# Optimization experiments

Hardware: AMD Instinct MI355X
Metric: run time of the kernel (lower is better)

## Reference

```python
import jax, jax.numpy as jnp
import numpy as np

K = 3           # kernel_size
PAD = 1         # padding
HEADS = 6
C = 192
CH = C // HEADS           # channels per head = 32
SCALE = CH ** (-0.5)
KK = K * K                # 9


def unfold3(x):
    # x: [N,C,H,W] -> [N,C,9,H,W] (im2col with k=3, pad=1, stride=1)
    N, c, H, W = x.shape
    xp = jnp.pad(x, ((0, 0), (0, 0), (PAD, PAD), (PAD, PAD)))
    return jnp.stack([xp[:, :, i:i + H, j:j + W] for i in range(K) for j in range(K)], axis=2)


def fold3(y):
    # y: [N,C,9,H,W] -> [N,C,H,W] (scatter-add inverse of unfold3)
    N, c, kk, H, W = y.shape
    out = jnp.zeros((N, c, H + 2 * PAD, W + 2 * PAD), dtype=y.dtype)
    idx = 0
    for i in range(K):
        for j in range(K):
            out = out.at[:, :, i:i + H, j:j + W].add(y[:, :, idx])
            idx += 1
    return out[:, :, PAD:PAD + H, PAD:PAD + W]


def setup_inputs() -> dict:
    key = jax.random.key(0)
    ks = jax.random.split(key, 6)
    N, H, W = 16, 56, 56
    s = 0.02
    return {
        "x": jax.random.normal(ks[0], (N, C, H, W), jnp.float32),
        "Wv": jax.random.normal(ks[1], (C, C), jnp.float32) * s,          # fc (no bias)
        "Wa": jax.random.normal(ks[2], (C, KK * KK * HEADS), jnp.float32) * s,  # fc_att weight
        "ba": jax.random.normal(ks[3], (KK * KK * HEADS,), jnp.float32) * s,
        "Wp": jax.random.normal(ks[4], (C, C), jnp.float32) * s,          # fc_proj weight
        "bp": jax.random.normal(ks[5], (C,), jnp.float32) * s,
    }


def reference(x, Wv, Wa, ba, Wp, bp):
    N, c, H, W = x.shape
    HW = H * W
    # value projection (pointwise linear over channels)
    v = jnp.einsum("nchw,cd->ndhw", x, Wv)
    # unfold values: [N,C,9,H,W] -> [N,heads,ch,9,HW] -> [N,heads,HW,9,ch]
    vu = unfold3(v).reshape(N, HEADS, CH, KK, HW).transpose(0, 1, 4, 3, 2)
    # attention logits from (avg-pooled, here identity since stride=1) input
    att = jnp.einsum("nchw,ck->nhwk", x, Wa) + ba       # [N,H,W,81*heads]
    att = att.reshape(N, HW, HEADS, KK, KK).transpose(0, 2, 1, 3, 4)  # [N,heads,HW,9,9]
    att = jax.nn.softmax(att * SCALE, axis=-1)          # dropout is identity at inference
    # apply per-position 9x9 attention to the 9 gathered neighbors
    out = jnp.einsum("nhpkl,nhplc->nhpkc", att, vu)      # [N,heads,HW,9,ch]
    # fold back: layout (heads, ch, kk) matches unfold layout (C, kk)
    out = out.transpose(0, 1, 4, 3, 2).reshape(N, c, KK, H, W)
    folded = fold3(out)                                  # [N,C,H,W]
    # output projection
    return jnp.einsum("nchw,cd->ndhw", folded, Wp) + bp[None, :, None, None]
```

## Files before the change

kernel.cpp:

```cpp
#include <hip/hip_runtime.h>
#include <hip/hip_bf16.h>
#include <math.h>

#define HW 3136
#define NC 192
#define NHEADS 6
#define IMG 56
#define NATT 486
#define YSTR 768
#define ATT_SCALE 0.17677669529663687f

typedef __attribute__((ext_vector_type(8))) short short8;
typedef __attribute__((ext_vector_type(8))) unsigned short ushort8;
typedef __attribute__((ext_vector_type(4))) float float4v;

__device__ __forceinline__ float bf2f(unsigned short u) {
    unsigned int x = ((unsigned int)u) << 16;
    return __builtin_bit_cast(float, x);
}
__device__ __forceinline__ unsigned short f2bf(float f) {
    __hip_bfloat16 h = __float2bfloat16(f);
    return __builtin_bit_cast(unsigned short, h);
}
__device__ __forceinline__ void gload_lds16(const void* g, void* l) {
    __builtin_amdgcn_global_load_lds((const __attribute__((address_space(1))) void*)g,
                                     (__attribute__((address_space(3))) void*)l, 16, 0, 0);
}

__global__ __launch_bounds__(256) void transpose_x(const float* __restrict__ x,
                                                   unsigned short* __restrict__ xt)
{
    __shared__ float tile[64][65];
    int bx = blockIdx.x;
    int n = (bx * 64) / HW;
    int hw0 = (bx * 64) % HW;
    int c0 = blockIdx.y * 64;
    int tl = threadIdx.x & 63, tg = threadIdx.x >> 6;
    const float* xn = x + (size_t)n * NC * HW;
#pragma unroll
    for (int i = 0; i < 16; ++i)
        tile[tg * 16 + i][tl] = xn[(size_t)(c0 + tg * 16 + i) * HW + hw0 + tl];
    __syncthreads();
    unsigned short* xp = xt + ((size_t)n * HW + hw0) * NC + c0;
#pragma unroll
    for (int i = 0; i < 16; ++i) {
        int hwr = tg * 16 + i;
        xp[(size_t)hwr * NC + tl] = f2bf(tile[tl][hwr]);
    }
}

__global__ __launch_bounds__(256) void prep_weights(
    const float* __restrict__ Wv, const float* __restrict__ Wa, const float* __restrict__ Wp,
    const float* __restrict__ ba,
    unsigned short* __restrict__ Wall, unsigned short* __restrict__ Wpt,
    float* __restrict__ ball)
{
    int idx = blockIdx.x * 256 + threadIdx.x;
    if (idx < 36864) {
        int d = idx / 192, k = idx - d * 192;
        Wpt[idx] = f2bf(Wp[(size_t)k * NC + d]);
    }
    if (idx < 147456) {
        int d = idx / 192, k = idx - d * 192;
        unsigned short val;
        float bv = 0.f;
        if (d < 192) {
            val = f2bf(Wv[(size_t)k * NC + d]);
        } else {
            int dp = d - 192;
            int head = dp / 96, rr = dp - head * 96;
            int k9 = rr / 10, l = rr - k9 * 10;
            bool valid = (k9 < 9) && (l < 9);
            int src = head * 81 + k9 * 9 + l;
            val = valid ? f2bf(Wa[(size_t)k * NATT + src]) : (unsigned short)0;
            bv = valid ? ba[src] : 0.f;
        }
        Wall[idx] = val;
        if (k == 0) ball[d] = bv;
    }
}

__global__ __launch_bounds__(256) void gemm_big(
    const unsigned short* __restrict__ A, const unsigned short* __restrict__ W,
    const float* __restrict__ ball, unsigned short* __restrict__ Y)
{
    __shared__ __align__(16) unsigned short As[2][4096];
    __shared__ __align__(16) unsigned short Bs[2][4096];
    int t = threadIdx.x, lane = t & 63, wave = t >> 6;
    int col0 = blockIdx.x * 128, row0 = blockIdx.y * 128;
    int fr = lane & 15, fq = lane >> 4;
    int wm = (wave >> 1) * 64, wn = (wave & 1) * 64;
    int srow = lane >> 2;
    int soff = (lane & 3) * 16;
    const char* Ab = (const char*)A;
    const char* Wb = (const char*)W;

    float4v acc[4][4] = {};

#define STAGE_BIG(buf, k0)                                                        \
    {                                                                             \
        _Pragma("unroll")                                                         \
        for (int i = 0; i < 2; ++i) {                                             \
            int j = wave * 2 + i;                                                 \
            gload_lds16(Ab + (size_t)(row0 + j * 16 + srow) * 384 + (k0)*2 + soff,\
                        (char*)As[buf] + j * 1024);                               \
            gload_lds16(Wb + (size_t)(col0 + j * 16 + srow) * 384 + (k0)*2 + soff,\
                        (char*)Bs[buf] + j * 1024);                               \
        }                                                                         \
    }

    STAGE_BIG(0, 0);
    for (int s = 0; s < 6; ++s) {
        if (s < 5) STAGE_BIG((s + 1) & 1, (s + 1) * 32);
        __syncthreads();
        int buf = s & 1;
        short8 af[4], bf[4];
#pragma unroll
        for (int mi = 0; mi < 4; ++mi)
            af[mi] = *(const short8*)((const char*)As[buf] + (wm + mi * 16 + fr) * 64 + fq * 16);
#pragma unroll
        for (int ni = 0; ni < 4; ++ni)
            bf[ni] = *(const short8*)((const char*)Bs[buf] + (wn + ni * 16 + fr) * 64 + fq * 16);
#pragma unroll
        for (int mi = 0; mi < 4; ++mi)
#pragma unroll
            for (int ni = 0; ni < 4; ++ni)
                acc[mi][ni] = __builtin_amdgcn_mfma_f32_16x16x32_bf16(
                    af[mi], bf[ni], acc[mi][ni], 0, 0, 0);
        __syncthreads();
    }

#pragma unroll
    for (int ni = 0; ni < 4; ++ni) {
        int col = col0 + wn + ni * 16 + fr;
        float b = ball[col];
#pragma unroll
        for (int mi = 0; mi < 4; ++mi) {
            int row = row0 + wm + mi * 16 + fq * 4;
#pragma unroll
            for (int r = 0; r < 4; ++r)
                Y[(size_t)(row + r) * YSTR + col] = f2bf(acc[mi][ni][r] + b);
        }
    }
#undef STAGE_BIG
}

__global__ __launch_bounds__(256) void gemm_small(
    const unsigned short* __restrict__ A,
    const unsigned short* __restrict__ B,
    const float* __restrict__ bias, float* __restrict__ out)
{
    __shared__ __align__(16) unsigned short As[2][2048];
    __shared__ __align__(16) unsigned short Bs[2][8192];
    int t = threadIdx.x, lane = t & 63, wave = t >> 6;
    int n0 = blockIdx.x * 256, m0 = blockIdx.y * 64;
    int fr = lane & 15, fq = lane >> 4;
    int srow = lane >> 2, soff = (lane & 3) * 16;
    const char* Ab = (const char*)A;
    const char* Bb = (const char*)B;

    float4v acc[4][4] = {};

#define STAGE_SMALL(buf, k0)                                                      \
    {                                                                             \
        gload_lds16(Ab + (size_t)(m0 + wave * 16 + srow) * 384 + (k0)*2 + soff,   \
                    (char*)As[buf] + wave * 1024);                                \
        _Pragma("unroll")                                                         \
        for (int i = 0; i < 4; ++i) {                                             \
            int j = wave * 4 + i;                                                 \
            gload_lds16(Bb + (size_t)(n0 + j * 16 + srow) * 384 + (k0)*2 + soff,  \
                        (char*)Bs[buf] + j * 1024);                               \
        }                                                                         \
    }

    STAGE_SMALL(0, 0);
    for (int s = 0; s < 6; ++s) {
        if (s < 5) STAGE_SMALL((s + 1) & 1, (s + 1) * 32);
        __syncthreads();
        int buf = s & 1;
        short8 af[4], bf[4];
#pragma unroll
        for (int mi = 0; mi < 4; ++mi)
            af[mi] = *(const short8*)((const char*)As[buf] + (mi * 16 + fr) * 64 + fq * 16);
#pragma unroll
        for (int ni = 0; ni < 4; ++ni)
            bf[ni] = *(const short8*)((const char*)Bs[buf] + (wave * 64 + ni * 16 + fr) * 64 + fq * 16);
#pragma unroll
        for (int mi = 0; mi < 4; ++mi)
#pragma unroll
            for (int ni = 0; ni < 4; ++ni)
                acc[mi][ni] = __builtin_amdgcn_mfma_f32_16x16x32_bf16(
                    af[mi], bf[ni], acc[mi][ni], 0, 0, 0);
        __syncthreads();
    }

#pragma unroll
    for (int ni = 0; ni < 4; ++ni) {
        int n = n0 + wave * 64 + ni * 16 + fr;
        int img = n / HW, phw = n - img * HW;
        float* op = out + (size_t)img * (NC * HW) + phw;
#pragma unroll
        for (int mi = 0; mi < 4; ++mi) {
            int m = m0 + mi * 16 + fq * 4;
#pragma unroll
            for (int r = 0; r < 4; ++r)
                op[(size_t)(m + r) * HW] = acc[mi][ni][r] + bias[m + r];
        }
    }
#undef STAGE_SMALL
}

__global__ __launch_bounds__(256) void fused_att_agg(
    const unsigned short* __restrict__ Y, unsigned short* __restrict__ fold)
{
    __shared__ float swc[192 * 25];
    int t = threadIdx.x;
    int pos_base = blockIdx.x * 32;

    if (t < 192) {
        int pos = t / 6, head = t - pos * 6;
        int rem = pos_base + pos;
        int hw = rem % HW;
        int h = hw / IMG, w = hw % IMG;
        const unsigned short* attn = Y + (size_t)rem * YSTR + 192 + head * 96;
        float wc[25];
#pragma unroll
        for (int d = 0; d < 25; ++d) wc[d] = 0.f;
#pragma unroll
        for (int k = 0; k < 9; ++k) {
            const int oky = k / 3 - 1, okx = k % 3 - 1;
            int hh = h - oky, ww = w - okx;
            if (hh < 0 || hh >= IMG || ww < 0 || ww >= IMG) continue;
            const unsigned short* ap = attn - (ptrdiff_t)(oky * IMG + okx) * YSTR + k * 10;
            ushort8 a8;
            __builtin_memcpy(&a8, ap, 16);
            float a[9];
#pragma unroll
            for (int l = 0; l < 8; ++l) a[l] = bf2f(a8[l]);
            a[8] = bf2f(ap[8]);
            float m = -1e30f;
#pragma unroll
            for (int l = 0; l < 9; ++l) m = fmaxf(m, a[l]);
            float s = 0.f;
#pragma unroll
            for (int l = 0; l < 9; ++l) {
                a[l] = __expf((a[l] - m) * ATT_SCALE);
                s += a[l];
            }
            float r = 1.f / s;
#pragma unroll
            for (int l = 0; l < 9; ++l) {
                const int dy = (l / 3 - 1) - oky + 2;
                const int dx = (l % 3 - 1) - okx + 2;
                wc[dy * 5 + dx] += a[l] * r;
            }
        }
        float* o = swc + t * 25;
#pragma unroll
        for (int d = 0; d < 25; ++d) o[d] = wc[d];
    }
    __syncthreads();

#pragma unroll
    for (int i = 0; i < 3; ++i) {
        int item = i * 256 + t;
        int pos = item / 24, sub = item - pos * 24;
        int head = sub >> 2, q8 = sub & 3;
        int rem = pos_base + pos;
        int hw = rem % HW;
        int h = hw / IMG, w = hw % IMG;
        const float* wp = swc + (pos * 6 + head) * 25;
        const unsigned short* vb = Y + (size_t)rem * YSTR + head * 32 + q8 * 8;
        float acc[8];
#pragma unroll
        for (int j = 0; j < 8; ++j) acc[j] = 0.f;
        if (h >= 2 && h < IMG - 2 && w >= 2 && w < IMG - 2) {
#pragma unroll
            for (int d = 0; d < 25; ++d) {
                const int dy = d / 5 - 2, dx = d % 5 - 2;
                float wf = wp[d];
                ushort8 vv = *(const ushort8*)(vb + (dy * IMG + dx) * YSTR);
#pragma unroll
                for (int j = 0; j < 8; ++j)
                    acc[j] += wf * bf2f(vv[j]);
            }
        } else {
#pragma unroll
            for (int d = 0; d < 25; ++d) {
                const int dy = d / 5 - 2, dx = d % 5 - 2;
                int hh = h + dy, ww = w + dx;
                bool ok = (hh >= 0) & (hh < IMG) & (ww >= 0) & (ww < IMG);
                float wf = ok ? wp[d] : 0.f;
                const unsigned short* vp = vb + (ok ? (dy * IMG + dx) * YSTR : 0);
                ushort8 vv = *(const ushort8*)vp;
#pragma unroll
                for (int j = 0; j < 8; ++j)
                    acc[j] += wf * bf2f(vv[j]);
            }
        }
        unsigned short* fo = fold + (size_t)rem * NC + head * 32 + q8 * 8;
        ushort8 ov;
#pragma unroll
        for (int j = 0; j < 8; ++j) ov[j] = f2bf(acc[j]);
        *(ushort8*)fo = ov;
    }
}

extern "C" void kernel_launch(void* const* d_in, const int* in_sizes, int n_in,
                              void* d_out, int out_size, void* d_ws, size_t ws_size,
                              hipStream_t stream)
{
    const float* x  = (const float*)d_in[0];
    const float* Wv = (const float*)d_in[1];
    const float* Wa = (const float*)d_in[2];
    const float* ba = (const float*)d_in[3];
    const float* Wp = (const float*)d_in[4];
    const float* bp = (const float*)d_in[5];
    float* out = (float*)d_out;

    unsigned short* xt    = (unsigned short*)d_ws;
    unsigned short* Y     = xt + 9633792;
    unsigned short* Wall  = Y + 38535168;
    unsigned short* Wpt   = Wall + 147456;
    float*          ball  = (float*)(Wpt + 36864);
    unsigned short* foldb = xt;

    dim3 blk(256);
    prep_weights<<<576, blk, 0, stream>>>(Wv, Wa, Wp, ba, Wall, Wpt, ball);
    transpose_x<<<dim3(784, 3), blk, 0, stream>>>(x, xt);
    gemm_big<<<dim3(6, 392), blk, 0, stream>>>(xt, Wall, ball, Y);
    fused_att_agg<<<1568, blk, 0, stream>>>(Y, foldb);
    gemm_small<<<dim3(196, 3), blk, 0, stream>>>(Wpt, foldb, bp, out);
}
```

Measured before the change: 210.0 us.

## Tile attention-aggregation by spatial patch per head with LDS-staged value halo

The fused attention-aggregation kernel now assigns each block an 8x28 spatial tile for a single head, instead of 32 linear positions across all heads. The block first stages a zero-padded 12x32 halo of that head's value vectors into shared memory. The 25-tap aggregation then reads from LDS instead of issuing repeated global loads, and the separate boundary path is no longer needed. This cuts redundant global/L2 traffic for overlapping neighborhoods. The cost is extra LDS use, which may lower occupancy, plus some halo overfetch.

```diff
diff --git a/kernel.cpp b/kernel.cpp
--- a/kernel.cpp
+++ b/kernel.cpp
@@ -213,16 +213,36 @@
 __global__ __launch_bounds__(256) void fused_att_agg(
     const unsigned short* __restrict__ Y, unsigned short* __restrict__ fold)
 {
-    __shared__ float swc[192 * 25];
+    __shared__ __align__(16) unsigned short vt[12 * 32 * 32];
+    __shared__ float swc[224 * 25];
     int t = threadIdx.x;
-    int pos_base = blockIdx.x * 32;
-
-    if (t < 192) {
-        int pos = t / 6, head = t - pos * 6;
-        int rem = pos_base + pos;
-        int hw = rem % HW;
-        int h = hw / IMG, w = hw % IMG;
-        const unsigned short* attn = Y + (size_t)rem * YSTR + 192 + head * 96;
+    int bid = blockIdx.x;
+    int head = bid % NHEADS; int tmp = bid / NHEADS;
+    int tcol = tmp & 1; tmp >>= 1;
+    int trow = tmp % 7; int img = tmp / 7;
+    int h0 = trow * 8, w0 = tcol * 28;
+
+    {
+        const unsigned short* Yv = Y + head * 32;
+#pragma unroll
+        for (int i = 0; i < 6; ++i) {
+            int u = i * 256 + t;
+            int slot = u >> 2, q = u & 3;
+            int vrow = slot >> 5, vcol = slot & 31;
+            int hh = h0 - 2 + vrow, ww = w0 - 2 + vcol;
+            bool ok = (hh >= 0) & (hh < IMG) & (ww >= 0) & (ww < IMG);
+            ushort8 val = {};
+            if (ok)
+                val = *(const ushort8*)(Yv + (size_t)(img * HW + hh * IMG + ww) * YSTR + q * 8);
+            *(ushort8*)&vt[(size_t)slot * 32 + q * 8] = val;
+        }
+    }
+
+    if (t < 224) {
+        int ph = t / 28, pw = t - (t / 28) * 28;
+        int h = h0 + ph, w = w0 + pw;
+        const unsigned short* attn =
+            Y + (size_t)(img * HW + h * IMG + w) * YSTR + 192 + head * 96;
         float wc[25];
 #pragma unroll
         for (int d = 0; d < 25; ++d) wc[d] = 0.f;
@@ -262,47 +282,31 @@
     __syncthreads();
 
 #pragma unroll
-    for (int i = 0; i < 3; ++i) {
+    for (int i = 0; i < 4; ++i) {
         int item = i * 256 + t;
-        int pos = item / 24, sub = item - pos * 24;
-        int head = sub >> 2, q8 = sub & 3;
-        int rem = pos_base + pos;
-        int hw = rem % HW;
-        int h = hw / IMG, w = hw % IMG;
-        const float* wp = swc + (pos * 6 + head) * 25;
-        const unsigned short* vb = Y + (size_t)rem * YSTR + head * 32 + q8 * 8;
-        float acc[8];
-#pragma unroll
-        for (int j = 0; j < 8; ++j) acc[j] = 0.f;
-        if (h >= 2 && h < IMG - 2 && w >= 2 && w < IMG - 2) {
+        if (item < 896) {
+            int p = item >> 2, q8 = item & 3;
+            int ph = p / 28, pw = p - (p / 28) * 28;
+            const float* wp = swc + p * 25;
+            float acc[8];
+#pragma unroll
+            for (int j = 0; j < 8; ++j) acc[j] = 0.f;
 #pragma unroll
             for (int d = 0; d < 25; ++d) {
-                const int dy = d / 5 - 2, dx = d % 5 - 2;
+                const int dy = d / 5, dx = d % 5;
                 float wf = wp[d];
-                ushort8 vv = *(const ushort8*)(vb + (dy * IMG + dx) * YSTR);
+                ushort8 vv = *(const ushort8*)&vt[(((ph + dy) << 5) + (pw + dx)) * 32 + q8 * 8];
 #pragma unroll
                 for (int j = 0; j < 8; ++j)
                     acc[j] += wf * bf2f(vv[j]);
             }
-        } else {
-#pragma unroll
-            for (int d = 0; d < 25; ++d) {
-                const int dy = d / 5 - 2, dx = d % 5 - 2;
-                int hh = h + dy, ww = w + dx;
-                bool ok = (hh >= 0) & (hh < IMG) & (ww >= 0) & (ww < IMG);
-                float wf = ok ? wp[d] : 0.f;
-                const unsigned short* vp = vb + (ok ? (dy * IMG + dx) * YSTR : 0);
-                ushort8 vv = *(const ushort8*)vp;
-#pragma unroll
-                for (int j = 0; j < 8; ++j)
-                    acc[j] += wf * bf2f(vv[j]);
-            }
-        }
-        unsigned short* fo = fold + (size_t)rem * NC + head * 32 + q8 * 8;
-        ushort8 ov;
-#pragma unroll
-        for (int j = 0; j < 8; ++j) ov[j] = f2bf(acc[j]);
-        *(ushort8*)fo = ov;
+            int rem = img * HW + (h0 + ph) * IMG + (w0 + pw);
+            unsigned short* fo = fold + (size_t)rem * NC + head * 32 + q8 * 8;
+            ushort8 ov;
+#pragma unroll
+            for (int j = 0; j < 8; ++j) ov[j] = f2bf(acc[j]);
+            *(ushort8*)fo = ov;
+        }
     }
 }
 
@@ -329,6 +333,6 @@
     prep_weights<<<576, blk, 0, stream>>>(Wv, Wa, Wp, ba, Wall, Wpt, ball);
     transpose_x<<<dim3(784, 3), blk, 0, stream>>>(x, xt);
     gemm_big<<<dim3(6, 392), blk, 0, stream>>>(xt, Wall, ball, Y);
-    fused_att_agg<<<1568, blk, 0, stream>>>(Y, foldb);
+    fused_att_agg<<<1344, blk, 0, stream>>>(Y, foldb);
     gemm_small<<<dim3(196, 3), blk, 0, stream>>>(Wpt, foldb, bp, out);
 }
```

Result: faster. 194.9 us (-7.2%).
